# Kernel optimization log

Measured on AMD Instinct MI355X. Metric: run time of the kernel, lower is better.

## Reference

```python
import jax, jax.numpy as jnp
import numpy as np

N = 50000          # nodes
E = 800000         # edges
F_IN = 64          # node_features (== LSTM hidden)
C = 100            # conv_out_channels of GatedGraphConv
T = 8              # n_target


def setup_inputs() -> dict:
    key = jax.random.key(0)
    ks = jax.random.split(key, 20)
    s = 0.05
    return {
        "x": jax.random.normal(ks[0], (N, F_IN), jnp.float32),
        "edge_index": jax.random.randint(ks[1], (2, E), 0, N, jnp.int64),
        "edge_weight": jax.random.uniform(ks[2], (E,), jnp.float32),
        "h_0": jax.random.normal(ks[3], (1, N, F_IN), jnp.float32),
        "c_0": jax.random.normal(ks[4], (1, N, F_IN), jnp.float32),
        # GatedGraphConv: weight [num_layers=1, C, C]
        "ggc_w": jax.random.normal(ks[5], (1, C, C), jnp.float32) * s,
        # GRUCell(C, C)
        "gru_w_ih": jax.random.normal(ks[6], (3 * C, C), jnp.float32) * s,
        "gru_w_hh": jax.random.normal(ks[7], (3 * C, C), jnp.float32) * s,
        "gru_b_ih": jnp.zeros((3 * C,), jnp.float32),
        "gru_b_hh": jnp.zeros((3 * C,), jnp.float32),
        # LSTM(input=C, hidden=F_IN, num_layers=1)
        "lstm_w_ih": jax.random.normal(ks[8], (4 * F_IN, C), jnp.float32) * s,
        "lstm_w_hh": jax.random.normal(ks[9], (4 * F_IN, F_IN), jnp.float32) * s,
        "lstm_b_ih": jnp.zeros((4 * F_IN,), jnp.float32),
        "lstm_b_hh": jnp.zeros((4 * F_IN,), jnp.float32),
        # final Linear(F_IN -> T)
        "lin_w": jax.random.normal(ks[10], (T, F_IN), jnp.float32) * s,
        "lin_b": jnp.zeros((T,), jnp.float32),
    }


def reference(x, edge_index, edge_weight, h_0, c_0,
              ggc_w, gru_w_ih, gru_w_hh, gru_b_ih, gru_b_hh,
              lstm_w_ih, lstm_w_hh, lstm_b_ih, lstm_b_hh, lin_w, lin_b):
    src, dst = edge_index[0], edge_index[1]
    # --- GatedGraphConv (1 layer, mean aggr) ---
    xp = jnp.pad(x, ((0, 0), (0, C - x.shape[1])))  # pad features to C
    m = xp @ ggc_w[0]                               # [N, C]
    msg = m[src] * edge_weight[:, None]             # [E, C] gather + weight
    summ = jax.ops.segment_sum(msg, dst, num_segments=N)
    cnt = jax.ops.segment_sum(jnp.ones_like(edge_weight), dst, num_segments=N)
    agg = summ / jnp.maximum(cnt, 1.0)[:, None]     # scatter-mean
    # GRUCell(agg, xp)
    gi = agg @ gru_w_ih.T + gru_b_ih
    gh = xp @ gru_w_hh.T + gru_b_hh
    i_r, i_z, i_n = jnp.split(gi, 3, axis=1)
    h_r, h_z, h_n = jnp.split(gh, 3, axis=1)
    r = jax.nn.sigmoid(i_r + h_r)
    z = jax.nn.sigmoid(i_z + h_z)
    n = jnp.tanh(i_n + r * h_n)
    conv_h = (1.0 - z) * n + z * xp                 # [N, C]
    # --- LSTM, one time step, batch=N, hidden=F_IN ---
    gates = conv_h @ lstm_w_ih.T + lstm_b_ih + h_0[0] @ lstm_w_hh.T + lstm_b_hh
    i_g, f_g, g_g, o_g = jnp.split(gates, 4, axis=1)
    i_g = jax.nn.sigmoid(i_g)
    f_g = jax.nn.sigmoid(f_g)
    g_g = jnp.tanh(g_g)
    o_g = jax.nn.sigmoid(o_g)
    c1 = f_g * c_0[0] + i_g * g_g                   # [N, F_IN]
    h1 = o_g * jnp.tanh(c1)                         # [N, F_IN]
    # --- relu + linear head ---
    out = jax.nn.relu(h1) @ lin_w.T + lin_b         # [N, T]
    return out, h1[None], c1[None]
```

## Files before the change

### kernel.cpp

```cpp
#include <hip/hip_runtime.h>

#define N_NODES 50000
#define N_EDGES 800000
#define F_INF   64
#define C_CH    100
#define T_OUT   8

typedef unsigned short u16;
typedef unsigned int   u32;
typedef __attribute__((ext_vector_type(8))) short bf16x8;
typedef __attribute__((ext_vector_type(4))) float f32x4;

__device__ __forceinline__ float sigmoidf_(float x) {
    return 1.0f / (1.0f + __expf(-x));
}
__device__ __forceinline__ float tanhf_(float x) {
    return 1.0f - 2.0f / (__expf(2.0f * x) + 1.0f);
}
__device__ __forceinline__ u16 f2bf(float f) {
    union { float f; u32 u; } v; v.f = f;
    u32 u = v.u;
    u += 0x7FFF + ((u >> 16) & 1);
    return (u16)(u >> 16);
}
__device__ __forceinline__ float bf2f(u16 h) {
    union { u32 u; float f; } v; v.u = ((u32)h) << 16;
    return v.f;
}
__device__ __forceinline__ float asf_(int i) {
    union { int i; float f; } v; v.i = i; return v.f;
}

#define XBF_B  1563
#define WG2_ELEMS (7 * 4 * 4 * 64 * 8)
#define WL2_ELEMS (4 * 6 * 4 * 64 * 8)
#define WP_B  ((WG2_ELEMS + WL2_ELEMS + 255) / 256)
__global__ void k_prep(const float* __restrict__ x,
                       const float* __restrict__ ggc, const float* __restrict__ gwih,
                       const float* __restrict__ gwhh,
                       const float* __restrict__ lwih, const float* __restrict__ lwhh,
                       u16* __restrict__ xbf,
                       u16* __restrict__ Wg2, u16* __restrict__ Wl2) {
    int gb = blockIdx.x;
    if (gb < XBF_B) {
        int idx = gb * 256 + threadIdx.x;
        if (idx >= N_NODES * F_INF / 8) return;
        float4 a = ((const float4*)x)[idx * 2];
        float4 b = ((const float4*)x)[idx * 2 + 1];
        uint4 p;
        p.x = (u32)f2bf(a.x) | ((u32)f2bf(a.y) << 16);
        p.y = (u32)f2bf(a.z) | ((u32)f2bf(a.w) << 16);
        p.z = (u32)f2bf(b.x) | ((u32)f2bf(b.y) << 16);
        p.w = (u32)f2bf(b.z) | ((u32)f2bf(b.w) << 16);
        ((uint4*)xbf)[idx] = p;
        return;
    }
    int idx = (gb - XBF_B) * 256 + threadIdx.x;
    if (idx < WG2_ELEMS) {
        int e    = idx & 7;
        int lane = (idx >> 3) & 63;
        int g    = (idx >> 9) & 3;
        int kt   = (idx >> 11) & 3;
        int ct   = idx >> 13;
        int c = ct * 16 + (lane & 15);
        int k = kt * 32 + (lane >> 4) * 8 + e;
        float val = 0.0f;
        if (c < 100) {
            if (g < 3) {
                if (k < 64) {
                    const float* wr = gwih + (g * 100 + c) * 100;
                    const float* gr = ggc + k * 100;
                    float s = 0.0f;
#pragma unroll 4
                    for (int j = 0; j < 100; ++j) s += wr[j] * gr[j];
                    val = s;
                } else if (g < 2) {
                    val = gwhh[(g * 100 + c) * 100 + (k - 64)];
                }
            } else {
                if (k >= 64) val = gwhh[(200 + c) * 100 + (k - 64)];
            }
        }
        Wg2[idx] = f2bf(val);
    } else if (idx < WG2_ELEMS + WL2_ELEMS) {
        int i2 = idx - WG2_ELEMS;
        int e    = i2 & 7;
        int lane = (i2 >> 3) & 63;
        int g    = (i2 >> 9) & 3;
        int ctkt = i2 >> 11;
        int ct = ctkt / 6, kt = ctkt - ct * 6;
        int c = ct * 16 + (lane & 15);
        int k = kt * 32 + (lane >> 4) * 8 + e;
        float val = 0.0f;
        if (k < 100) val = lwih[(g * 64 + c) * 100 + k];
        else if (k >= 128) val = lwhh[(g * 64 + c) * 64 + (k - 128)];
        Wl2[i2] = f2bf(val);
    }
}

#define BK_NPB 64
#define BK_NB  ((N_NODES + BK_NPB - 1) / BK_NPB)
#define BCAP   1280
#define PART_T     1024
#define PART_CHUNK 8192
#define PART_B ((N_EDGES + PART_CHUNK - 1) / PART_CHUNK)
#define PART_LDS_SIZE 110880
__global__ __launch_bounds__(PART_T, 4) void k_part(const int* __restrict__ ei,
                                                    const float* __restrict__ ew,
                                                    int* __restrict__ bcur,
                                                    int2* __restrict__ bucket) {
    extern __shared__ __align__(16) char pls[];
    int2* se    = (int2*)pls;
    int*  gdst  = (int*)(pls + 65536);
    int*  hist  = (int*)(pls + 98304);
    int*  ebase = (int*)(pls + 101432);
    int*  cur   = (int*)(pls + 104560);
    int*  gbase = (int*)(pls + 107688);
    int*  wsum  = (int*)(pls + 110816);
    int tid = threadIdx.x;
    int e0 = blockIdx.x * PART_CHUNK;
    int cnt = N_EDGES - e0;
    if (cnt > PART_CHUNK) cnt = PART_CHUNK;

    for (int i = tid; i < BK_NB; i += PART_T) hist[i] = 0;
    __syncthreads();

    int srcr[8], dstr[8]; float wvr[8];
#pragma unroll
    for (int k = 0; k < 8; ++k) {
        int e = tid + k * PART_T;
        if (e < cnt) {
            srcr[k] = ei[e0 + e];
            dstr[k] = ei[N_EDGES + e0 + e];
            wvr[k]  = ew[e0 + e];
            atomicAdd(&hist[dstr[k] >> 6], 1);
        } else dstr[k] = -1;
    }
    __syncthreads();

    {
        int lane = tid & 63, w = tid >> 6;
        int h = (tid < BK_NB) ? hist[tid] : 0;
        int v = h;
#pragma unroll
        for (int off = 1; off < 64; off <<= 1) {
            int u = __shfl_up(v, off, 64);
            if (lane >= off) v += u;
        }
        if (lane == 63) wsum[w] = v;
        __syncthreads();
        if (tid < 16) {
            int s = wsum[tid];
#pragma unroll
            for (int off = 1; off < 16; off <<= 1) {
                int u = __shfl_up(s, off, 16);
                if (tid >= off) s += u;
            }
            wsum[tid] = s;
        }
        __syncthreads();
        if (tid < BK_NB) {
            int v2 = v + ((w > 0) ? wsum[w - 1] : 0);
            int ex = v2 - h;
            ebase[tid] = ex;
            cur[tid] = ex;
            gbase[tid] = (h > 0) ? atomicAdd(&bcur[tid * 16], h) : 0;
        }
    }
    __syncthreads();

#pragma unroll
    for (int k = 0; k < 8; ++k) {
        if (dstr[k] >= 0) {
            int b = dstr[k] >> 6;
            int p = atomicAdd(&cur[b], 1);
            int gl = gbase[b] + (p - ebase[b]);
            se[p] = make_int2(srcr[k] | ((dstr[k] & 63) << 16), __float_as_int(wvr[k]));
            gdst[p] = (gl < BCAP) ? (b * BCAP + gl) : -1;
        }
    }
    __syncthreads();

    for (int i = tid; i < cnt; i += PART_T) {
        int g = gdst[i];
        if (g >= 0) bucket[g] = se[i];
    }
}

__global__ __launch_bounds__(512, 3) void k_bagg(
    const int2* __restrict__ bucket, const int* __restrict__ bcur,
    const u16* __restrict__ xbf, u16* __restrict__ xaggbf) {
    __shared__ int2 se[BCAP];
    __shared__ int  hist[64];
    __shared__ int  base[65];
    __shared__ int  cur[64];
    int tid = threadIdx.x;
    int b = blockIdx.x;
    int n0 = b * BK_NPB;

    if (tid < 64) hist[tid] = 0;
    __syncthreads();

    int cnt = bcur[b * 16];
    if (cnt > BCAP) cnt = BCAP;
    const int2* mybkt = bucket + (size_t)b * BCAP;

    int2 r0 = make_int2(0, 0), r1 = make_int2(0, 0), r2 = make_int2(0, 0);
    int nr = 0;
    if (tid < cnt)        { r0 = mybkt[tid];        atomicAdd(&hist[(r0.x >> 16) & 63], 1); nr = 1; }
    if (tid + 512 < cnt)  { r1 = mybkt[tid + 512];  atomicAdd(&hist[(r1.x >> 16) & 63], 1); nr = 2; }
    if (tid + 1024 < cnt) { r2 = mybkt[tid + 1024]; atomicAdd(&hist[(r2.x >> 16) & 63], 1); nr = 3; }
    __syncthreads();

    if (tid < 64) {
        int h = hist[tid];
        int v = h;
#pragma unroll
        for (int off = 1; off < 64; off <<= 1) {
            int u = __shfl_up(v, off, 64);
            if (tid >= off) v += u;
        }
        base[tid + 1] = v;
        if (tid == 0) base[0] = 0;
        cur[tid] = v - h;
    }
    __syncthreads();

    if (nr > 0) { int p = atomicAdd(&cur[(r0.x >> 16) & 63], 1); se[p] = r0; }
    if (nr > 1) { int p = atomicAdd(&cur[(r1.x >> 16) & 63], 1); se[p] = r1; }
    if (nr > 2) { int p = atomicAdd(&cur[(r2.x >> 16) & 63], 1); se[p] = r2; }
    __syncthreads();

    int w = tid >> 6, lane = tid & 63;
#pragma unroll
    for (int j = 0; j < 8; ++j) {
        int nl = w * 8 + j;
        int s = base[nl], epos = base[nl + 1];
        float acc = 0.0f;
        int i = s;
        for (; i + 3 < epos; i += 4) {
            int2 e0 = se[i], e1 = se[i + 1], e2 = se[i + 2], e3 = se[i + 3];
            float v0 = bf2f(xbf[(size_t)(e0.x & 0xFFFF) * 64 + lane]);
            float v1 = bf2f(xbf[(size_t)(e1.x & 0xFFFF) * 64 + lane]);
            float v2 = bf2f(xbf[(size_t)(e2.x & 0xFFFF) * 64 + lane]);
            float v3 = bf2f(xbf[(size_t)(e3.x & 0xFFFF) * 64 + lane]);
            acc += v0 * asf_(e0.y); acc += v1 * asf_(e1.y);
            acc += v2 * asf_(e2.y); acc += v3 * asf_(e3.y);
        }
        for (; i < epos; ++i) {
            int2 e0 = se[i];
            acc += bf2f(xbf[(size_t)(e0.x & 0xFFFF) * 64 + lane]) * asf_(e0.y);
        }
        int n = n0 + nl;
        if (n < N_NODES) {
            acc /= fmaxf((float)(epos - s), 1.0f);
            xaggbf[(size_t)n * 64 + lane] = f2bf(acc);
        }
    }
}

#define RNN_A2   19456
#define RNN_BIAS 47104
#define RNN_BL   49504
#define RNN_LWF  50528
#define RNN_LBS  52576
__global__ __launch_bounds__(256, 3) void k_rnn(
    const u16* __restrict__ xaggbf, const u16* __restrict__ xbf,
    const float* __restrict__ h0, const float* __restrict__ c0,
    const u16* __restrict__ Wg2, const u16* __restrict__ Wl2,
    const float* __restrict__ gbih, const float* __restrict__ gbhh,
    const float* __restrict__ lbih, const float* __restrict__ lbhh,
    const float* __restrict__ lw, const float* __restrict__ lb,
    float* __restrict__ out, float* __restrict__ h1, float* __restrict__ c1) {
    __shared__ __align__(16) char smem[52608];
    u16*   A1   = (u16*)(smem);
    u16*   A2   = (u16*)(smem + RNN_A2);
    float* bias = (float*)(smem + RNN_BIAS);
    float* bl   = (float*)(smem + RNN_BL);
    float* lwf  = (float*)(smem + RNN_LWF);
    float* lbs  = (float*)(smem + RNN_LBS);
    float* h1s  = (float*)(smem);
    int tid = threadIdx.x;
    int n0 = blockIdx.x * 64;

    for (int i = tid; i < 1024; i += 256) {
        int row = i >> 4, ch = i & 15;
        int n = n0 + row;
        uint4 v = make_uint4(0, 0, 0, 0);
        if (n < N_NODES)
            v = (ch < 8) ? ((const uint4*)xaggbf)[n * 8 + ch]
                         : ((const uint4*)xbf)[n * 8 + (ch - 8)];
        *(uint4*)(A1 + row * 152 + ch * 8) = v;
    }
    for (int i = tid; i < 512; i += 256) {
        int row = i >> 3, ch = i & 7;
        int n = n0 + row;
        uint4 p = make_uint4(0, 0, 0, 0);
        if (n < N_NODES) {
            float4 f0 = ((const float4*)h0)[n * 16 + ch * 2];
            float4 f1 = ((const float4*)h0)[n * 16 + ch * 2 + 1];
            p.x = (u32)f2bf(f0.x) | ((u32)f2bf(f0.y) << 16);
            p.y = (u32)f2bf(f0.z) | ((u32)f2bf(f0.w) << 16);
            p.z = (u32)f2bf(f1.x) | ((u32)f2bf(f1.y) << 16);
            p.w = (u32)f2bf(f1.z) | ((u32)f2bf(f1.w) << 16);
        }
        *(uint4*)(A2 + row * 216 + 128 + ch * 8) = p;
    }
    for (int i = tid; i < 128; i += 256) {
        int row = i >> 1, ch = i & 1;
        *(uint4*)(A2 + row * 216 + 112 + ch * 8) = make_uint4(0, 0, 0, 0);
    }
    for (int i = tid; i < 600; i += 256)
        bias[i] = (i < 300) ? gbih[i] : gbhh[i - 300];
    if (tid < 256) bl[tid] = lbih[tid] + lbhh[tid];
    for (int i = tid; i < 512; i += 256) {
        int k = i >> 3, t = i & 7;
        lwf[i] = lw[t * F_INF + k];
    }
    if (tid < 8) lbs[tid] = lb[tid];
    __syncthreads();

    int w = tid >> 6, lane = tid & 63, quad = lane >> 4, ln = lane & 15;

    for (int ct = w; ct < 7; ct += 4) {
        bf16x8 wb[4][4];
#pragma unroll
        for (int kt = 0; kt < 4; ++kt)
#pragma unroll
            for (int g = 0; g < 4; ++g)
                wb[kt][g] = ((const bf16x8*)Wg2)[((ct * 4 + kt) * 4 + g) * 64 + lane];
        int c = ct * 16 + ln;
        float br = 0.f, bz = 0.f, bn2 = 0.f, bh2 = 0.f;
        if (c < 100) {
            br  = bias[c]       + bias[300 + c];
            bz  = bias[100 + c] + bias[400 + c];
            bn2 = bias[200 + c];
            bh2 = bias[500 + c];
        }
#pragma unroll
        for (int mtp = 0; mtp < 2; ++mtp) {
            f32x4 ar[2], az[2], an[2], ah[2];
#pragma unroll
            for (int mt = 0; mt < 2; ++mt) {
                ar[mt] = (f32x4){0.f, 0.f, 0.f, 0.f};
                az[mt] = ar[mt]; an[mt] = ar[mt]; ah[mt] = ar[mt];
            }
#pragma unroll
            for (int kt = 0; kt < 4; ++kt) {
#pragma unroll
                for (int mt = 0; mt < 2; ++mt) {
                    bf16x8 a = *(const bf16x8*)(A1 + (mtp * 32 + mt * 16 + ln) * 152 + kt * 32 + quad * 8);
                    ar[mt] = __builtin_amdgcn_mfma_f32_16x16x32_bf16(a, wb[kt][0], ar[mt], 0, 0, 0);
                    az[mt] = __builtin_amdgcn_mfma_f32_16x16x32_bf16(a, wb[kt][1], az[mt], 0, 0, 0);
                    an[mt] = __builtin_amdgcn_mfma_f32_16x16x32_bf16(a, wb[kt][2], an[mt], 0, 0, 0);
                    ah[mt] = __builtin_amdgcn_mfma_f32_16x16x32_bf16(a, wb[kt][3], ah[mt], 0, 0, 0);
                }
            }
#pragma unroll
            for (int mt = 0; mt < 2; ++mt) {
#pragma unroll
                for (int reg = 0; reg < 4; ++reg) {
                    int m = mtp * 32 + mt * 16 + quad * 4 + reg;
                    float val = 0.0f;
                    if (c < 100) {
                        float rv = sigmoidf_(ar[mt][reg] + br);
                        float zv = sigmoidf_(az[mt][reg] + bz);
                        float nv = tanhf_(an[mt][reg] + bn2 + rv * (ah[mt][reg] + bh2));
                        float xp = (c < F_INF) ? bf2f(A1[m * 152 + 64 + c]) : 0.0f;
                        val = (1.0f - zv) * nv + zv * xp;
                    }
                    A2[m * 216 + c] = f2bf(val);
                }
            }
        }
    }
    __syncthreads();

    float h1v[2][2][4];
    {
        int ct = w;
        int c = ct * 16 + ln;
        float bi = bl[c], bff = bl[64 + c], bg = bl[128 + c], bo = bl[192 + c];
#pragma unroll
        for (int mtp = 0; mtp < 2; ++mtp) {
            f32x4 ai[2], af[2], ag[2], ao[2];
#pragma unroll
            for (int mt = 0; mt < 2; ++mt) {
                ai[mt] = (f32x4){0.f, 0.f, 0.f, 0.f};
                af[mt] = ai[mt]; ag[mt] = ai[mt]; ao[mt] = ai[mt];
            }
            {
                bf16x8 wbh[3][4];
#pragma unroll
                for (int kt = 0; kt < 3; ++kt)
#pragma unroll
                    for (int g = 0; g < 4; ++g)
                        wbh[kt][g] = ((const bf16x8*)Wl2)[((ct * 6 + kt) * 4 + g) * 64 + lane];
#pragma unroll
                for (int kt = 0; kt < 3; ++kt) {
#pragma unroll
                    for (int mt = 0; mt < 2; ++mt) {
                        bf16x8 a = *(const bf16x8*)(A2 + (mtp * 32 + mt * 16 + ln) * 216 + kt * 32 + quad * 8);
                        ai[mt] = __builtin_amdgcn_mfma_f32_16x16x32_bf16(a, wbh[kt][0], ai[mt], 0, 0, 0);
                        af[mt] = __builtin_amdgcn_mfma_f32_16x16x32_bf16(a, wbh[kt][1], af[mt], 0, 0, 0);
                        ag[mt] = __builtin_amdgcn_mfma_f32_16x16x32_bf16(a, wbh[kt][2], ag[mt], 0, 0, 0);
                        ao[mt] = __builtin_amdgcn_mfma_f32_16x16x32_bf16(a, wbh[kt][3], ao[mt], 0, 0, 0);
                    }
                }
            }
            {
                bf16x8 wbh[3][4];
#pragma unroll
                for (int kt = 0; kt < 3; ++kt)
#pragma unroll
                    for (int g = 0; g < 4; ++g)
                        wbh[kt][g] = ((const bf16x8*)Wl2)[((ct * 6 + kt + 3) * 4 + g) * 64 + lane];
#pragma unroll
                for (int kt = 0; kt < 3; ++kt) {
#pragma unroll
                    for (int mt = 0; mt < 2; ++mt) {
                        bf16x8 a = *(const bf16x8*)(A2 + (mtp * 32 + mt * 16 + ln) * 216 + (kt + 3) * 32 + quad * 8);
                        ai[mt] = __builtin_amdgcn_mfma_f32_16x16x32_bf16(a, wbh[kt][0], ai[mt], 0, 0, 0);
                        af[mt] = __builtin_amdgcn_mfma_f32_16x16x32_bf16(a, wbh[kt][1], af[mt], 0, 0, 0);
                        ag[mt] = __builtin_amdgcn_mfma_f32_16x16x32_bf16(a, wbh[kt][2], ag[mt], 0, 0, 0);
                        ao[mt] = __builtin_amdgcn_mfma_f32_16x16x32_bf16(a, wbh[kt][3], ao[mt], 0, 0, 0);
                    }
                }
            }
#pragma unroll
            for (int mt = 0; mt < 2; ++mt) {
#pragma unroll
                for (int reg = 0; reg < 4; ++reg) {
                    int m = mtp * 32 + mt * 16 + quad * 4 + reg;
                    int n = n0 + m;
                    float iv = sigmoidf_(ai[mt][reg] + bi);
                    float fv = sigmoidf_(af[mt][reg] + bff);
                    float gv = tanhf_(ag[mt][reg] + bg);
                    float ov = sigmoidf_(ao[mt][reg] + bo);
                    float c0v = (n < N_NODES) ? c0[(size_t)n * F_INF + c] : 0.0f;
                    float cc = fv * c0v + iv * gv;
                    float hh = ov * tanhf_(cc);
                    h1v[mtp][mt][reg] = hh;
                    if (n < N_NODES) {
                        c1[(size_t)n * F_INF + c] = cc;
                        h1[(size_t)n * F_INF + c] = hh;
                    }
                }
            }
        }
    }
    __syncthreads();

    {
        int c = w * 16 + ln;
#pragma unroll
        for (int mtp = 0; mtp < 2; ++mtp)
#pragma unroll
            for (int mt = 0; mt < 2; ++mt)
#pragma unroll
                for (int reg = 0; reg < 4; ++reg) {
                    int m = mtp * 32 + mt * 16 + quad * 4 + reg;
                    h1s[m * 65 + c] = h1v[mtp][mt][reg];
                }
    }
    __syncthreads();

    for (int o = tid; o < 512; o += 256) {
        int nl = o & 63, t = o >> 6;
        float acc = lbs[t];
        const float* hr = h1s + nl * 65;
#pragma unroll 8
        for (int k = 0; k < F_INF; ++k)
            acc += fmaxf(hr[k], 0.0f) * lwf[k * 8 + t];
        int n = n0 + nl;
        if (n < N_NODES) out[(size_t)n * T_OUT + t] = acc;
    }
}

extern "C" void kernel_launch(void* const* d_in, const int* in_sizes, int n_in,
                              void* d_out, int out_size, void* d_ws, size_t ws_size,
                              hipStream_t stream) {
    const float* x     = (const float*)d_in[0];
    const int*   ei    = (const int*)d_in[1];
    const float* ew    = (const float*)d_in[2];
    const float* h0    = (const float*)d_in[3];
    const float* c0    = (const float*)d_in[4];
    const float* ggc   = (const float*)d_in[5];
    const float* gwih  = (const float*)d_in[6];
    const float* gwhh  = (const float*)d_in[7];
    const float* gbih  = (const float*)d_in[8];
    const float* gbhh  = (const float*)d_in[9];
    const float* lwih  = (const float*)d_in[10];
    const float* lwhh  = (const float*)d_in[11];
    const float* lbih  = (const float*)d_in[12];
    const float* lbhh  = (const float*)d_in[13];
    const float* lw    = (const float*)d_in[14];
    const float* lb    = (const float*)d_in[15];

    float* out = (float*)d_out;
    float* h1  = out + (size_t)N_NODES * T_OUT;
    float* c1  = h1 + (size_t)N_NODES * F_INF;

    char* ws = (char*)d_ws;
    u16*   xaggbf = (u16*)ws;
    u16*   xbf    = (u16*)(ws + 6400000);
    u16*   Wg2    = (u16*)(ws + 12800000);
    u16*   Wl2    = (u16*)(ws + 12914688);
    int2*  bucket = (int2*)(ws + 13012992);
    int*   bcur   = (int*)(ws + 21020672);

    static int lds_ok = 0;
    if (!lds_ok) {
        hipFuncSetAttribute((const void*)k_part,
                            hipFuncAttributeMaxDynamicSharedMemorySize, PART_LDS_SIZE);
        lds_ok = 1;
    }

    hipMemsetAsync(bcur, 0, BK_NB * 16 * sizeof(int), stream);

    k_prep<<<XBF_B + WP_B, 256, 0, stream>>>(
        x, ggc, gwih, gwhh, lwih, lwhh, xbf, Wg2, Wl2);
    k_part<<<PART_B, PART_T, PART_LDS_SIZE, stream>>>(ei, ew, bcur, bucket);
    k_bagg<<<BK_NB, 512, 0, stream>>>(bucket, bcur, xbf, xaggbf);
    { int b = (N_NODES + 63) / 64;
      k_rnn<<<b, 256, 0, stream>>>(xaggbf, xbf, h0, c0, Wg2, Wl2,
                                   gbih, gbhh, lbih, lbhh, lw, lb,
                                   out, h1, c1); }
}
```

Baseline: 205.4 us.

## Merge prep and partition kernels; halve RNN tile to raise occupancy

Combines the bf16 conversion/weight-packing kernel and the edge-partition kernel into a single launch, with block ranges dispatched by blockIdx and 1024-thread blocks throughout. This removes one launch and lets the two independent jobs overlap. The fused RNN kernel now handles 32 nodes per block instead of 64, shrinking LDS so occupancy can rise from 3 to 5 blocks, and c0 is prefetched into registers at kernel start. In exchange, the per-node weight fragment loads are amortised over fewer rows and twice as many blocks are launched.

```diff
diff --git a/kernel.cpp b/kernel.cpp
--- a/kernel.cpp
+++ b/kernel.cpp
@@ -31,19 +31,110 @@
     union { int i; float f; } v; v.i = i; return v.f;
 }
 
-#define XBF_B  1563
+#define BK_NPB 64
+#define BK_NB  ((N_NODES + BK_NPB - 1) / BK_NPB)
+#define BCAP   1280
+#define PART_T     1024
+#define PART_CHUNK 8192
+#define PART_B ((N_EDGES + PART_CHUNK - 1) / PART_CHUNK)
+#define PP_XBF_B 391
 #define WG2_ELEMS (7 * 4 * 4 * 64 * 8)
 #define WL2_ELEMS (4 * 6 * 4 * 64 * 8)
-#define WP_B  ((WG2_ELEMS + WL2_ELEMS + 255) / 256)
-__global__ void k_prep(const float* __restrict__ x,
-                       const float* __restrict__ ggc, const float* __restrict__ gwih,
-                       const float* __restrict__ gwhh,
-                       const float* __restrict__ lwih, const float* __restrict__ lwhh,
-                       u16* __restrict__ xbf,
-                       u16* __restrict__ Wg2, u16* __restrict__ Wl2) {
+#define PP_W_B ((WG2_ELEMS + WL2_ELEMS) / 1024)
+#define PP_B (PART_B + PP_XBF_B + PP_W_B)
+#define PP_LDS_SIZE 110880
+__global__ __launch_bounds__(PART_T) void k_pp(
+    const int* __restrict__ ei, const float* __restrict__ ew,
+    const float* __restrict__ x,
+    const float* __restrict__ ggc, const float* __restrict__ gwih,
+    const float* __restrict__ gwhh,
+    const float* __restrict__ lwih, const float* __restrict__ lwhh,
+    int* __restrict__ bcur, int2* __restrict__ bucket,
+    u16* __restrict__ xbf, u16* __restrict__ Wg2, u16* __restrict__ Wl2) {
+    extern __shared__ __align__(16) char pls[];
     int gb = blockIdx.x;
-    if (gb < XBF_B) {
-        int idx = gb * 256 + threadIdx.x;
+    int tid = threadIdx.x;
+
+    if (gb < PART_B) {
+        int2* se    = (int2*)pls;
+        int*  gdst  = (int*)(pls + 65536);
+        int*  hist  = (int*)(pls + 98304);
+        int*  ebase = (int*)(pls + 101432);
+        int*  cur   = (int*)(pls + 104560);
+        int*  gbase = (int*)(pls + 107688);
+        int*  wsum  = (int*)(pls + 110816);
+        int e0 = gb * PART_CHUNK;
+        int cnt = N_EDGES - e0;
+        if (cnt > PART_CHUNK) cnt = PART_CHUNK;
+
+        for (int i = tid; i < BK_NB; i += PART_T) hist[i] = 0;
+        __syncthreads();
+
+        int srcr[8], dstr[8]; float wvr[8];
+#pragma unroll
+        for (int k = 0; k < 8; ++k) {
+            int e = tid + k * PART_T;
+            if (e < cnt) {
+                srcr[k] = ei[e0 + e];
+                dstr[k] = ei[N_EDGES + e0 + e];
+                wvr[k]  = ew[e0 + e];
+                atomicAdd(&hist[dstr[k] >> 6], 1);
+            } else dstr[k] = -1;
+        }
+        __syncthreads();
+
+        {
+            int lane = tid & 63, w = tid >> 6;
+            int h = (tid < BK_NB) ? hist[tid] : 0;
+            int v = h;
+#pragma unroll
+            for (int off = 1; off < 64; off <<= 1) {
+                int u = __shfl_up(v, off, 64);
+                if (lane >= off) v += u;
+            }
+            if (lane == 63) wsum[w] = v;
+            __syncthreads();
+            if (tid < 16) {
+                int s = wsum[tid];
+#pragma unroll
+                for (int off = 1; off < 16; off <<= 1) {
+                    int u = __shfl_up(s, off, 16);
+                    if (tid >= off) s += u;
+                }
+                wsum[tid] = s;
+            }
+            __syncthreads();
+            if (tid < BK_NB) {
+                int v2 = v + ((w > 0) ? wsum[w - 1] : 0);
+                int ex = v2 - h;
+                ebase[tid] = ex;
+                cur[tid] = ex;
+                gbase[tid] = (h > 0) ? atomicAdd(&bcur[tid * 16], h) : 0;
+            }
+        }
+        __syncthreads();
+
+#pragma unroll
+        for (int k = 0; k < 8; ++k) {
+            if (dstr[k] >= 0) {
+                int b = dstr[k] >> 6;
+                int p = atomicAdd(&cur[b], 1);
+                int gl = gbase[b] + (p - ebase[b]);
+                se[p] = make_int2(srcr[k] | ((dstr[k] & 63) << 16), __float_as_int(wvr[k]));
+                gdst[p] = (gl < BCAP) ? (b * BCAP + gl) : -1;
+            }
+        }
+        __syncthreads();
+
+        for (int i = tid; i < cnt; i += PART_T) {
+            int g = gdst[i];
+            if (g >= 0) bucket[g] = se[i];
+        }
+        return;
+    }
+
+    if (gb < PART_B + PP_XBF_B) {
+        int idx = (gb - PART_B) * 1024 + tid;
         if (idx >= N_NODES * F_INF / 8) return;
         float4 a = ((const float4*)x)[idx * 2];
         float4 b = ((const float4*)x)[idx * 2 + 1];
@@ -55,7 +146,8 @@
         ((uint4*)xbf)[idx] = p;
         return;
     }
-    int idx = (gb - XBF_B) * 256 + threadIdx.x;
+
+    int idx = (gb - PART_B - PP_XBF_B) * 1024 + tid;
     if (idx < WG2_ELEMS) {
         int e    = idx & 7;
         int lane = (idx >> 3) & 63;
@@ -98,95 +190,6 @@
     }
 }
 
-#define BK_NPB 64
-#define BK_NB  ((N_NODES + BK_NPB - 1) / BK_NPB)
-#define BCAP   1280
-#define PART_T     1024
-#define PART_CHUNK 8192
-#define PART_B ((N_EDGES + PART_CHUNK - 1) / PART_CHUNK)
-#define PART_LDS_SIZE 110880
-__global__ __launch_bounds__(PART_T, 4) void k_part(const int* __restrict__ ei,
-                                                    const float* __restrict__ ew,
-                                                    int* __restrict__ bcur,
-                                                    int2* __restrict__ bucket) {
-    extern __shared__ __align__(16) char pls[];
-    int2* se    = (int2*)pls;
-    int*  gdst  = (int*)(pls + 65536);
-    int*  hist  = (int*)(pls + 98304);
-    int*  ebase = (int*)(pls + 101432);
-    int*  cur   = (int*)(pls + 104560);
-    int*  gbase = (int*)(pls + 107688);
-    int*  wsum  = (int*)(pls + 110816);
-    int tid = threadIdx.x;
-    int e0 = blockIdx.x * PART_CHUNK;
-    int cnt = N_EDGES - e0;
-    if (cnt > PART_CHUNK) cnt = PART_CHUNK;
-
-    for (int i = tid; i < BK_NB; i += PART_T) hist[i] = 0;
-    __syncthreads();
-
-    int srcr[8], dstr[8]; float wvr[8];
-#pragma unroll
-    for (int k = 0; k < 8; ++k) {
-        int e = tid + k * PART_T;
-        if (e < cnt) {
-            srcr[k] = ei[e0 + e];
-            dstr[k] = ei[N_EDGES + e0 + e];
-            wvr[k]  = ew[e0 + e];
-            atomicAdd(&hist[dstr[k] >> 6], 1);
-        } else dstr[k] = -1;
-    }
-    __syncthreads();
-
-    {
-        int lane = tid & 63, w = tid >> 6;
-        int h = (tid < BK_NB) ? hist[tid] : 0;
-        int v = h;
-#pragma unroll
-        for (int off = 1; off < 64; off <<= 1) {
-            int u = __shfl_up(v, off, 64);
-            if (lane >= off) v += u;
-        }
-        if (lane == 63) wsum[w] = v;
-        __syncthreads();
-        if (tid < 16) {
-            int s = wsum[tid];
-#pragma unroll
-            for (int off = 1; off < 16; off <<= 1) {
-                int u = __shfl_up(s, off, 16);
-                if (tid >= off) s += u;
-            }
-            wsum[tid] = s;
-        }
-        __syncthreads();
-        if (tid < BK_NB) {
-            int v2 = v + ((w > 0) ? wsum[w - 1] : 0);
-            int ex = v2 - h;
-            ebase[tid] = ex;
-            cur[tid] = ex;
-            gbase[tid] = (h > 0) ? atomicAdd(&bcur[tid * 16], h) : 0;
-        }
-    }
-    __syncthreads();
-
-#pragma unroll
-    for (int k = 0; k < 8; ++k) {
-        if (dstr[k] >= 0) {
-            int b = dstr[k] >> 6;
-            int p = atomicAdd(&cur[b], 1);
-            int gl = gbase[b] + (p - ebase[b]);
-            se[p] = make_int2(srcr[k] | ((dstr[k] & 63) << 16), __float_as_int(wvr[k]));
-            gdst[p] = (gl < BCAP) ? (b * BCAP + gl) : -1;
-        }
-    }
-    __syncthreads();
-
-    for (int i = tid; i < cnt; i += PART_T) {
-        int g = gdst[i];
-        if (g >= 0) bucket[g] = se[i];
-    }
-}
-
 __global__ __launch_bounds__(512, 3) void k_bagg(
     const int2* __restrict__ bucket, const int* __restrict__ bcur,
     const u16* __restrict__ xbf, u16* __restrict__ xaggbf) {
@@ -259,12 +262,12 @@
     }
 }
 
-#define RNN_A2   19456
-#define RNN_BIAS 47104
-#define RNN_BL   49504
-#define RNN_LWF  50528
-#define RNN_LBS  52576
-__global__ __launch_bounds__(256, 3) void k_rnn(
+#define RNN_A2   9728
+#define RNN_BIAS 23552
+#define RNN_BL   25952
+#define RNN_LWF  26976
+#define RNN_LBS  29024
+__global__ __launch_bounds__(256, 5) void k_rnn(
     const u16* __restrict__ xaggbf, const u16* __restrict__ xbf,
     const float* __restrict__ h0, const float* __restrict__ c0,
     const u16* __restrict__ Wg2, const u16* __restrict__ Wl2,
@@ -272,7 +275,7 @@
     const float* __restrict__ lbih, const float* __restrict__ lbhh,
     const float* __restrict__ lw, const float* __restrict__ lb,
     float* __restrict__ out, float* __restrict__ h1, float* __restrict__ c1) {
-    __shared__ __align__(16) char smem[52608];
+    __shared__ __align__(16) char smem[29056];
     u16*   A1   = (u16*)(smem);
     u16*   A2   = (u16*)(smem + RNN_A2);
     float* bias = (float*)(smem + RNN_BIAS);
@@ -281,9 +284,21 @@
     float* lbs  = (float*)(smem + RNN_LBS);
     float* h1s  = (float*)(smem);
     int tid = threadIdx.x;
-    int n0 = blockIdx.x * 64;
-
-    for (int i = tid; i < 1024; i += 256) {
+    int n0 = blockIdx.x * 32;
+    int w = tid >> 6, lane = tid & 63, quad = lane >> 4, ln = lane & 15;
+
+    float c0r[2][4];
+    {
+        int c = w * 16 + ln;
+#pragma unroll
+        for (int mt = 0; mt < 2; ++mt)
+#pragma unroll
+            for (int reg = 0; reg < 4; ++reg) {
+                int n = n0 + mt * 16 + quad * 4 + reg;
+                c0r[mt][reg] = (n < N_NODES) ? c0[(size_t)n * F_INF + c] : 0.0f;
+            }
+    }
+    for (int i = tid; i < 512; i += 256) {
         int row = i >> 4, ch = i & 15;
         int n = n0 + row;
         uint4 v = make_uint4(0, 0, 0, 0);
@@ -292,8 +307,8 @@
                          : ((const uint4*)xbf)[n * 8 + (ch - 8)];
         *(uint4*)(A1 + row * 152 + ch * 8) = v;
     }
-    for (int i = tid; i < 512; i += 256) {
-        int row = i >> 3, ch = i & 7;
+    {
+        int row = tid >> 3, ch = tid & 7;
         int n = n0 + row;
         uint4 p = make_uint4(0, 0, 0, 0);
         if (n < N_NODES) {
@@ -306,9 +321,9 @@
         }
         *(uint4*)(A2 + row * 216 + 128 + ch * 8) = p;
     }
-    for (int i = tid; i < 128; i += 256) {
-        int row = i >> 1, ch = i & 1;
-        *(uint4*)(A2 + row * 216 + 112 + ch * 8) = make_uint4(0, 0, 0, 0);
+    if (tid < 64) {
+        int row = tid >> 1, ch2 = tid & 1;
+        *(uint4*)(A2 + row * 216 + 112 + ch2 * 8) = make_uint4(0, 0, 0, 0);
     }
     for (int i = tid; i < 600; i += 256)
         bias[i] = (i < 300) ? gbih[i] : gbhh[i - 300];
@@ -319,8 +334,6 @@
     }
     if (tid < 8) lbs[tid] = lb[tid];
     __syncthreads();
-
-    int w = tid >> 6, lane = tid & 63, quad = lane >> 4, ln = lane & 15;
 
     for (int ct = w; ct < 7; ct += 4) {
         bf16x8 wb[4][4];
@@ -337,114 +350,107 @@
             bn2 = bias[200 + c];
             bh2 = bias[500 + c];
         }
-#pragma unroll
-        for (int mtp = 0; mtp < 2; ++mtp) {
-            f32x4 ar[2], az[2], an[2], ah[2];
+        f32x4 ar[2], az[2], an[2], ah[2];
+#pragma unroll
+        for (int mt = 0; mt < 2; ++mt) {
+            ar[mt] = (f32x4){0.f, 0.f, 0.f, 0.f};
+            az[mt] = ar[mt]; an[mt] = ar[mt]; ah[mt] = ar[mt];
+        }
+#pragma unroll
+        for (int kt = 0; kt < 4; ++kt) {
 #pragma unroll
             for (int mt = 0; mt < 2; ++mt) {
-                ar[mt] = (f32x4){0.f, 0.f, 0.f, 0.f};
-                az[mt] = ar[mt]; an[mt] = ar[mt]; ah[mt] = ar[mt];
-            }
-#pragma unroll
-            for (int kt = 0; kt < 4; ++kt) {
-#pragma unroll
-                for (int mt = 0; mt < 2; ++mt) {
-                    bf16x8 a = *(const bf16x8*)(A1 + (mtp * 32 + mt * 16 + ln) * 152 + kt * 32 + quad * 8);
-                    ar[mt] = __builtin_amdgcn_mfma_f32_16x16x32_bf16(a, wb[kt][0], ar[mt], 0, 0, 0);
-                    az[mt] = __builtin_amdgcn_mfma_f32_16x16x32_bf16(a, wb[kt][1], az[mt], 0, 0, 0);
-                    an[mt] = __builtin_amdgcn_mfma_f32_16x16x32_bf16(a, wb[kt][2], an[mt], 0, 0, 0);
-                    ah[mt] = __builtin_amdgcn_mfma_f32_16x16x32_bf16(a, wb[kt][3], ah[mt], 0, 0, 0);
+                bf16x8 a = *(const bf16x8*)(A1 + (mt * 16 + ln) * 152 + kt * 32 + quad * 8);
+                ar[mt] = __builtin_amdgcn_mfma_f32_16x16x32_bf16(a, wb[kt][0], ar[mt], 0, 0, 0);
+                az[mt] = __builtin_amdgcn_mfma_f32_16x16x32_bf16(a, wb[kt][1], az[mt], 0, 0, 0);
+                an[mt] = __builtin_amdgcn_mfma_f32_16x16x32_bf16(a, wb[kt][2], an[mt], 0, 0, 0);
+                ah[mt] = __builtin_amdgcn_mfma_f32_16x16x32_bf16(a, wb[kt][3], ah[mt], 0, 0, 0);
+            }
+        }
+#pragma unroll
+        for (int mt = 0; mt < 2; ++mt) {
+#pragma unroll
+            for (int reg = 0; reg < 4; ++reg) {
+                int m = mt * 16 + quad * 4 + reg;
+                float val = 0.0f;
+                if (c < 100) {
+                    float rv = sigmoidf_(ar[mt][reg] + br);
+                    float zv = sigmoidf_(az[mt][reg] + bz);
+                    float nv = tanhf_(an[mt][reg] + bn2 + rv * (ah[mt][reg] + bh2));
+                    float xp = (c < F_INF) ? bf2f(A1[m * 152 + 64 + c]) : 0.0f;
+                    val = (1.0f - zv) * nv + zv * xp;
                 }
-            }
-#pragma unroll
-            for (int mt = 0; mt < 2; ++mt) {
-#pragma unroll
-                for (int reg = 0; reg < 4; ++reg) {
-                    int m = mtp * 32 + mt * 16 + quad * 4 + reg;
-                    float val = 0.0f;
-                    if (c < 100) {
-                        float rv = sigmoidf_(ar[mt][reg] + br);
-                        float zv = sigmoidf_(az[mt][reg] + bz);
-                        float nv = tanhf_(an[mt][reg] + bn2 + rv * (ah[mt][reg] + bh2));
-                        float xp = (c < F_INF) ? bf2f(A1[m * 152 + 64 + c]) : 0.0f;
-                        val = (1.0f - zv) * nv + zv * xp;
-                    }
-                    A2[m * 216 + c] = f2bf(val);
-                }
-            }
-        }
-    }
-    __syncthreads();
-
-    float h1v[2][2][4];
+                A2[m * 216 + c] = f2bf(val);
+            }
+        }
+    }
+    __syncthreads();
+
+    float h1v[2][4];
     {
         int ct = w;
         int c = ct * 16 + ln;
         float bi = bl[c], bff = bl[64 + c], bg = bl[128 + c], bo = bl[192 + c];
-#pragma unroll
-        for (int mtp = 0; mtp < 2; ++mtp) {
-            f32x4 ai[2], af[2], ag[2], ao[2];
-#pragma unroll
-            for (int mt = 0; mt < 2; ++mt) {
-                ai[mt] = (f32x4){0.f, 0.f, 0.f, 0.f};
-                af[mt] = ai[mt]; ag[mt] = ai[mt]; ao[mt] = ai[mt];
-            }
-            {
-                bf16x8 wbh[3][4];
-#pragma unroll
-                for (int kt = 0; kt < 3; ++kt)
-#pragma unroll
-                    for (int g = 0; g < 4; ++g)
-                        wbh[kt][g] = ((const bf16x8*)Wl2)[((ct * 6 + kt) * 4 + g) * 64 + lane];
-#pragma unroll
-                for (int kt = 0; kt < 3; ++kt) {
-#pragma unroll
-                    for (int mt = 0; mt < 2; ++mt) {
-                        bf16x8 a = *(const bf16x8*)(A2 + (mtp * 32 + mt * 16 + ln) * 216 + kt * 32 + quad * 8);
-                        ai[mt] = __builtin_amdgcn_mfma_f32_16x16x32_bf16(a, wbh[kt][0], ai[mt], 0, 0, 0);
-                        af[mt] = __builtin_amdgcn_mfma_f32_16x16x32_bf16(a, wbh[kt][1], af[mt], 0, 0, 0);
-                        ag[mt] = __builtin_amdgcn_mfma_f32_16x16x32_bf16(a, wbh[kt][2], ag[mt], 0, 0, 0);
-                        ao[mt] = __builtin_amdgcn_mfma_f32_16x16x32_bf16(a, wbh[kt][3], ao[mt], 0, 0, 0);
-                    }
+        f32x4 ai[2], af[2], ag[2], ao[2];
+#pragma unroll
+        for (int mt = 0; mt < 2; ++mt) {
+            ai[mt] = (f32x4){0.f, 0.f, 0.f, 0.f};
+            af[mt] = ai[mt]; ag[mt] = ai[mt]; ao[mt] = ai[mt];
+        }
+        {
+            bf16x8 wbh[3][4];
+#pragma unroll
+            for (int kt = 0; kt < 3; ++kt)
+#pragma unroll
+                for (int g = 0; g < 4; ++g)
+                    wbh[kt][g] = ((const bf16x8*)Wl2)[((ct * 6 + kt) * 4 + g) * 64 + lane];
+#pragma unroll
+            for (int kt = 0; kt < 3; ++kt) {
+#pragma unroll
+                for (int mt = 0; mt < 2; ++mt) {
+                    bf16x8 a = *(const bf16x8*)(A2 + (mt * 16 + ln) * 216 + kt * 32 + quad * 8);
+                    ai[mt] = __builtin_amdgcn_mfma_f32_16x16x32_bf16(a, wbh[kt][0], ai[mt], 0, 0, 0);
+                    af[mt] = __builtin_amdgcn_mfma_f32_16x16x32_bf16(a, wbh[kt][1], af[mt], 0, 0, 0);
+                    ag[mt] = __builtin_amdgcn_mfma_f32_16x16x32_bf16(a, wbh[kt][2], ag[mt], 0, 0, 0);
+                    ao[mt] = __builtin_amdgcn_mfma_f32_16x16x32_bf16(a, wbh[kt][3], ao[mt], 0, 0, 0);
                 }
             }
-            {
-                bf16x8 wbh[3][4];
-#pragma unroll
-                for (int kt = 0; kt < 3; ++kt)
-#pragma unroll
-                    for (int g = 0; g < 4; ++g)
-                        wbh[kt][g] = ((const bf16x8*)Wl2)[((ct * 6 + kt + 3) * 4 + g) * 64 + lane];
-#pragma unroll
-                for (int kt = 0; kt < 3; ++kt) {
-#pragma unroll
-                    for (int mt = 0; mt < 2; ++mt) {
-                        bf16x8 a = *(const bf16x8*)(A2 + (mtp * 32 + mt * 16 + ln) * 216 + (kt + 3) * 32 + quad * 8);
-                        ai[mt] = __builtin_amdgcn_mfma_f32_16x16x32_bf16(a, wbh[kt][0], ai[mt], 0, 0, 0);
-                        af[mt] = __builtin_amdgcn_mfma_f32_16x16x32_bf16(a, wbh[kt][1], af[mt], 0, 0, 0);
-                        ag[mt] = __builtin_amdgcn_mfma_f32_16x16x32_bf16(a, wbh[kt][2], ag[mt], 0, 0, 0);
-                        ao[mt] = __builtin_amdgcn_mfma_f32_16x16x32_bf16(a, wbh[kt][3], ao[mt], 0, 0, 0);
-                    }
+        }
+        {
+            bf16x8 wbh[3][4];
+#pragma unroll
+            for (int kt = 0; kt < 3; ++kt)
+#pragma unroll
+                for (int g = 0; g < 4; ++g)
+                    wbh[kt][g] = ((const bf16x8*)Wl2)[((ct * 6 + kt + 3) * 4 + g) * 64 + lane];
+#pragma unroll
+            for (int kt = 0; kt < 3; ++kt) {
+#pragma unroll
+                for (int mt = 0; mt < 2; ++mt) {
+                    bf16x8 a = *(const bf16x8*)(A2 + (mt * 16 + ln) * 216 + (kt + 3) * 32 + quad * 8);
+                    ai[mt] = __builtin_amdgcn_mfma_f32_16x16x32_bf16(a, wbh[kt][0], ai[mt], 0, 0, 0);
+                    af[mt] = __builtin_amdgcn_mfma_f32_16x16x32_bf16(a, wbh[kt][1], af[mt], 0, 0, 0);
+                    ag[mt] = __builtin_amdgcn_mfma_f32_16x16x32_bf16(a, wbh[kt][2], ag[mt], 0, 0, 0);
+                    ao[mt] = __builtin_amdgcn_mfma_f32_16x16x32_bf16(a, wbh[kt][3], ao[mt], 0, 0, 0);
                 }
             }
-#pragma unroll
-            for (int mt = 0; mt < 2; ++mt) {
-#pragma unroll
-                for (int reg = 0; reg < 4; ++reg) {
-                    int m = mtp * 32 + mt * 16 + quad * 4 + reg;
-                    int n = n0 + m;
-                    float iv = sigmoidf_(ai[mt][reg] + bi);
-                    float fv = sigmoidf_(af[mt][reg] + bff);
-                    float gv = tanhf_(ag[mt][reg] + bg);
-                    float ov = sigmoidf_(ao[mt][reg] + bo);
-                    float c0v = (n < N_NODES) ? c0[(size_t)n * F_INF + c] : 0.0f;
-                    float cc = fv * c0v + iv * gv;
-                    float hh = ov * tanhf_(cc);
-                    h1v[mtp][mt][reg] = hh;
-                    if (n < N_NODES) {
-                        c1[(size_t)n * F_INF + c] = cc;
-                        h1[(size_t)n * F_INF + c] = hh;
-                    }
+        }
+#pragma unroll
+        for (int mt = 0; mt < 2; ++mt) {
+#pragma unroll
+            for (int reg = 0; reg < 4; ++reg) {
+                int m = mt * 16 + quad * 4 + reg;
+                int n = n0 + m;
+                float iv = sigmoidf_(ai[mt][reg] + bi);
+                float fv = sigmoidf_(af[mt][reg] + bff);
+                float gv = tanhf_(ag[mt][reg] + bg);
+                float ov = sigmoidf_(ao[mt][reg] + bo);
+                float cc = fv * c0r[mt][reg] + iv * gv;
+                float hh = ov * tanhf_(cc);
+                h1v[mt][reg] = hh;
+                if (n < N_NODES) {
+                    c1[(size_t)n * F_INF + c] = cc;
+                    h1[(size_t)n * F_INF + c] = hh;
                 }
             }
         }
@@ -454,19 +460,17 @@
     {
         int c = w * 16 + ln;
 #pragma unroll
-        for (int mtp = 0; mtp < 2; ++mtp)
-#pragma unroll
-            for (int mt = 0; mt < 2; ++mt)
-#pragma unroll
-                for (int reg = 0; reg < 4; ++reg) {
-                    int m = mtp * 32 + mt * 16 + quad * 4 + reg;
-                    h1s[m * 65 + c] = h1v[mtp][mt][reg];
-                }
-    }
-    __syncthreads();
-
-    for (int o = tid; o < 512; o += 256) {
-        int nl = o & 63, t = o >> 6;
+        for (int mt = 0; mt < 2; ++mt)
+#pragma unroll
+            for (int reg = 0; reg < 4; ++reg) {
+                int m = mt * 16 + quad * 4 + reg;
+                h1s[m * 65 + c] = h1v[mt][reg];
+            }
+    }
+    __syncthreads();
+
+    {
+        int nl = tid & 31, t = tid >> 5;
         float acc = lbs[t];
         const float* hr = h1s + nl * 65;
 #pragma unroll 8
@@ -511,18 +515,17 @@
 
     static int lds_ok = 0;
     if (!lds_ok) {
-        hipFuncSetAttribute((const void*)k_part,
-                            hipFuncAttributeMaxDynamicSharedMemorySize, PART_LDS_SIZE);
+        hipFuncSetAttribute((const void*)k_pp,
+                            hipFuncAttributeMaxDynamicSharedMemorySize, PP_LDS_SIZE);
         lds_ok = 1;
     }
 
     hipMemsetAsync(bcur, 0, BK_NB * 16 * sizeof(int), stream);
 
-    k_prep<<<XBF_B + WP_B, 256, 0, stream>>>(
-        x, ggc, gwih, gwhh, lwih, lwhh, xbf, Wg2, Wl2);
-    k_part<<<PART_B, PART_T, PART_LDS_SIZE, stream>>>(ei, ew, bcur, bucket);
+    k_pp<<<PP_B, PART_T, PP_LDS_SIZE, stream>>>(
+        ei, ew, x, ggc, gwih, gwhh, lwih, lwhh, bcur, bucket, xbf, Wg2, Wl2);
     k_bagg<<<BK_NB, 512, 0, stream>>>(bucket, bcur, xbf, xaggbf);
-    { int b = (N_NODES + 63) / 64;
+    { int b = (N_NODES + 31) / 32;
       k_rnn<<<b, 256, 0, stream>>>(xaggbf, xbf, h0, c0, Wg2, Wl2,
                                    gbih, gbhh, lbih, lbhh, lw, lb,
                                    out, h1, c1); }
```

Result: slower. 210.5 us (+2.5%).
